# Kernel tuning notes

Hardware: AMD Instinct MI355X
Metric: run time of the kernel (lower is better)

## Reference

```python
import jax, jax.numpy as jnp
import numpy as np

B, S, D_MODEL = 4, 2048, 1024
N_HEAD, D_K, D_V = 16, 64, 64
LN_EPS = 1e-5


def setup_inputs() -> dict:
    key = jax.random.key(0)
    ks = jax.random.split(key, 8)
    std_qk = np.sqrt(2.0 / (D_MODEL + D_K)).astype(np.float32)
    std_v = np.sqrt(2.0 / (D_MODEL + D_V)).astype(np.float32)
    return {
        "q": jax.random.normal(ks[0], (B, S, D_MODEL), dtype=jnp.float32),
        "k": jax.random.normal(ks[1], (B, S, D_MODEL), dtype=jnp.float32),
        "v": jax.random.normal(ks[2], (B, S, D_MODEL), dtype=jnp.float32),
        "attn_mask": jax.random.randint(ks[3], (B, 1, S), 0, 2) > 0,
        # torch Linear weights: (out_features, in_features)
        "w_q": jax.random.normal(ks[4], (N_HEAD * D_K, D_MODEL), dtype=jnp.float32) * std_qk,
        "w_k": jax.random.normal(ks[5], (N_HEAD * D_K, D_MODEL), dtype=jnp.float32) * std_qk,
        "w_v": jax.random.normal(ks[6], (N_HEAD * D_V, D_MODEL), dtype=jnp.float32) * std_v,
        "w_fc": jax.random.normal(ks[7], (D_MODEL, N_HEAD * D_V), dtype=jnp.float32) * np.sqrt(2.0 / (D_MODEL + N_HEAD * D_V)).astype(np.float32),
        "ln_gamma": jnp.ones((D_MODEL,), dtype=jnp.float32),
        "ln_beta": jnp.zeros((D_MODEL,), dtype=jnp.float32),
    }


def _layer_norm(x, gamma, beta):
    mu = jnp.mean(x, axis=-1, keepdims=True)
    var = jnp.mean(jnp.square(x - mu), axis=-1, keepdims=True)
    return (x - mu) * jax.lax.rsqrt(var + LN_EPS) * gamma + beta


def reference(q, k, v, attn_mask, w_q, w_k, w_v, w_fc, ln_gamma, ln_beta):
    b, sq, _ = q.shape
    residual = q
    qh = (q @ w_q.T).reshape(b, sq, N_HEAD, D_K)          # [b,sq,h,dk]
    kh = (k @ w_k.T).reshape(b, -1, N_HEAD, D_K)          # [b,sk,h,dk]
    vh = (v @ w_v.T).reshape(b, -1, N_HEAD, D_V)          # [b,sk,h,dv]
    temperature = jnp.asarray(np.power(D_K, 0.5), dtype=q.dtype)
    scores = jnp.einsum("bqhd,bkhd->bhqk", qh, kh) / temperature
    # attn_mask: [b,1,sk] key-padding mask, True = masked
    scores = jnp.where(attn_mask[:, None, :, :], jnp.asarray(-1e6, scores.dtype), scores)
    attn = jax.nn.softmax(scores, axis=-1)                 # dropout is identity in eval
    out = jnp.einsum("bhqk,bkhd->bqhd", attn, vh).reshape(b, sq, N_HEAD * D_V)
    out = out @ w_fc.T
    out = _layer_norm(out + residual, ln_gamma, ln_beta)
    return out, attn
```

## Files before the change

kernel.cpp:

```cpp
#include <hip/hip_runtime.h>
#include <cstdint>
#include <cstddef>

#define B_  4
#define S_  2048
#define DM_ 1024
#define H_  16

typedef _Float16 h8 __attribute__((ext_vector_type(8)));
typedef _Float16 h4 __attribute__((ext_vector_type(4)));
typedef float f32x4 __attribute__((ext_vector_type(4)));

#define MFMA16(A_, B2_, C_) __builtin_amdgcn_mfma_f32_16x16x32_f16((A_), (B2_), (C_), 0, 0, 0)

__device__ __forceinline__ void gload_lds16(const void* g, void* l) {
  __builtin_amdgcn_global_load_lds(
      (const __attribute__((address_space(1))) unsigned int*)g,
      (__attribute__((address_space(3))) unsigned int*)l, 16, 0, 0);
}

template <int MODE, int A16>
__global__ __launch_bounds__(256, 2)
void gemm_bt(const void* __restrict__ Ap, const void* __restrict__ Wp,
             void* __restrict__ outp, int M, int N, int K) {
  __shared__ _Float16 As[128 * 32];
  __shared__ _Float16 Bs[128 * 32];
  const int tid = threadIdx.x;
  const int w = tid >> 6, lane = tid & 63;
  const int g = lane >> 4, li = lane & 15;
  const int wr = w >> 1, wc = w & 1;
  const int mBase = blockIdx.y * 128, nBase = blockIdx.x * 128;

  f32x4 acc[4][4] = {};

  _Float16* lA = As + w * 1024;
  _Float16* lB = Bs + w * 1024;

  const _Float16* gA16 =
      (const _Float16*)Ap + (size_t)(mBase + w * 32 + (lane >> 2)) * K + (lane & 3) * 8;
  const float* gA32 =
      (const float*)Ap + (size_t)(mBase + w * 32 + (lane >> 3)) * K + (lane & 7) * 4;
  const float* gW =
      (const float*)Wp + (size_t)(nBase + w * 32 + (lane >> 3)) * K + (lane & 7) * 4;

  for (int kt = 0; kt < K; kt += 32) {
    if (kt) __syncthreads();
    if constexpr (A16) {
      gload_lds16(gA16 + kt, lA);
      gload_lds16(gA16 + kt + (size_t)16 * K, lA + 512);
    } else {
#pragma unroll
      for (int it = 0; it < 4; ++it) {
        f32x4 v = *(const f32x4*)(gA32 + kt + (size_t)(it * 8) * K);
        h4 o;
        o[0] = (_Float16)v[0]; o[1] = (_Float16)v[1];
        o[2] = (_Float16)v[2]; o[3] = (_Float16)v[3];
        *(h4*)&lA[(it * 8 + (lane >> 3)) * 32 + (lane & 7) * 4] = o;
      }
    }
#pragma unroll
    for (int it = 0; it < 4; ++it) {
      f32x4 v = *(const f32x4*)(gW + kt + (size_t)(it * 8) * K);
      h4 o;
      o[0] = (_Float16)v[0]; o[1] = (_Float16)v[1];
      o[2] = (_Float16)v[2]; o[3] = (_Float16)v[3];
      *(h4*)&lB[(it * 8 + (lane >> 3)) * 32 + (lane & 7) * 4] = o;
    }
    __syncthreads();
    h8 af[4], bf[4];
#pragma unroll
    for (int t = 0; t < 4; ++t) af[t] = *(const h8*)&As[(wr * 64 + t * 16 + li) * 32 + g * 8];
#pragma unroll
    for (int u = 0; u < 4; ++u) bf[u] = *(const h8*)&Bs[(wc * 64 + u * 16 + li) * 32 + g * 8];
#pragma unroll
    for (int t = 0; t < 4; ++t)
#pragma unroll
      for (int u = 0; u < 4; ++u) acc[t][u] = MFMA16(af[t], bf[u], acc[t][u]);
  }

#pragma unroll
  for (int t = 0; t < 4; ++t) {
    const int grow0 = mBase + wr * 64 + t * 16 + g * 4;
#pragma unroll
    for (int u = 0; u < 4; ++u) {
      const int gcol = nBase + wc * 64 + u * 16 + li;
      if (MODE == 2) {
        float* o = (float*)outp;
#pragma unroll
        for (int r = 0; r < 4; ++r) o[(size_t)(grow0 + r) * N + gcol] = acc[t][u][r];
      } else if (MODE == 0) {
        _Float16* o = (_Float16*)outp;
        const int hh = gcol >> 6, d = gcol & 63;
#pragma unroll
        for (int r = 0; r < 4; ++r) {
          const int grow = grow0 + r;
          const int bb = grow >> 11, ss = grow & 2047;
          o[((size_t)((bb * H_ + hh) * S_ + ss)) * 64 + d] = (_Float16)acc[t][u][r];
        }
      } else {
        _Float16* o = (_Float16*)outp;
        const int hh = gcol >> 6, d = gcol & 63;
        const int bb = grow0 >> 11, ss = grow0 & 2047;
        h4 vv;
#pragma unroll
        for (int r = 0; r < 4; ++r) vv[r] = (_Float16)acc[t][u][r];
        *(h4*)&o[((size_t)((bb * H_ + hh) * 64 + d)) * S_ + ss] = vv;
      }
    }
  }
}

__global__ __launch_bounds__(256, 6)
void qk1_kernel(const _Float16* __restrict__ qh, const _Float16* __restrict__ kh,
                const int* __restrict__ mask, float* __restrict__ rlws) {
  __shared__ _Float16 sbias[S_];
  __shared__ __align__(16) _Float16 Ks[128 * 72];
  const int tid = threadIdx.x;
  const int w = tid >> 6, lane = tid & 63;
  const int g = lane >> 4, li = lane & 15;
  const int id = blockIdx.x;
  const int hh = id & 15, bb = (id >> 4) & 3, qt = id >> 6;
  const size_t bhS = ((size_t)bb * H_ + hh) * S_;
  const _Float16* khb = kh + bhS * 64;

  {
    const int4* mi = (const int4*)(mask + (size_t)bb * S_);
    int4 m0 = mi[tid * 2];
    int4 m1 = mi[tid * 2 + 1];
    _Float16* d = sbias + tid * 8;
    d[0] = m0.x ? (_Float16)-60000.f : (_Float16)-10.f;
    d[1] = m0.y ? (_Float16)-60000.f : (_Float16)-10.f;
    d[2] = m0.z ? (_Float16)-60000.f : (_Float16)-10.f;
    d[3] = m0.w ? (_Float16)-60000.f : (_Float16)-10.f;
    d[4] = m1.x ? (_Float16)-60000.f : (_Float16)-10.f;
    d[5] = m1.y ? (_Float16)-60000.f : (_Float16)-10.f;
    d[6] = m1.z ? (_Float16)-60000.f : (_Float16)-10.f;
    d[7] = m1.w ? (_Float16)-60000.f : (_Float16)-10.f;
  }

  h8 aq[2][2];
#pragma unroll
  for (int t = 0; t < 2; ++t) {
    const _Float16* qp = qh + (bhS + qt * 128 + w * 32 + t * 16 + li) * 64;
    aq[t][0] = *(const h8*)(qp + g * 8);
    aq[t][1] = *(const h8*)(qp + 32 + g * 8);
  }

  const int srow = tid >> 3;
  const int ssl = tid & 7;

  float l[2][4] = {};
  for (int kc = 0; kc < 16; ++kc) {
    __syncthreads();
#pragma unroll
    for (int rnd = 0; rnd < 4; ++rnd) {
      const int row = rnd * 32 + srow;
      const h8 kv = *(const h8*)(khb + (size_t)(kc * 128 + row) * 64 + ssl * 8);
      *(h8*)&Ks[row * 72 + ssl * 8] = kv;
    }
    __syncthreads();
    for (int kk = 0; kk < 8; ++kk) {
      const int krow = kk * 16 + li;
      const h8 bk0 = *(const h8*)&Ks[krow * 72 + g * 8];
      const h8 bk1 = *(const h8*)&Ks[krow * 72 + 32 + g * 8];
      const float bias = (float)sbias[kc * 128 + krow];
#pragma unroll
      for (int t = 0; t < 2; ++t) {
        f32x4 a = {0.f, 0.f, 0.f, 0.f};
        a = MFMA16(aq[t][0], bk0, a);
        a = MFMA16(aq[t][1], bk1, a);
#pragma unroll
        for (int r = 0; r < 4; ++r) l[t][r] += __expf(fmaf(a[r], 0.125f, bias));
      }
    }
  }

#pragma unroll
  for (int t = 0; t < 2; ++t)
#pragma unroll
    for (int r = 0; r < 4; ++r) {
      float s = l[t][r];
      s += __shfl_xor(s, 1);
      s += __shfl_xor(s, 2);
      s += __shfl_xor(s, 4);
      s += __shfl_xor(s, 8);
      if (li == 0)
        rlws[bhS + qt * 128 + w * 32 + t * 16 + g * 4 + r] = 1.0f / s;
    }
}

__global__ __launch_bounds__(256, 2)
void qk2_kernel(const _Float16* __restrict__ qh, const _Float16* __restrict__ kh,
                const _Float16* __restrict__ vt, const int* __restrict__ mask,
                const float* __restrict__ rlws, float* __restrict__ attn_out,
                _Float16* __restrict__ ctx) {
  __shared__ _Float16 sbias[S_];
  __shared__ __align__(16) _Float16 Pst[4][16 * 264];
  __shared__ __align__(16) _Float16 Ku[256 * 72];
  const int tid = threadIdx.x;
  const int w = tid >> 6, lane = tid & 63;
  const int g = lane >> 4, li = lane & 15;
  const int id = blockIdx.x;
  const int hh = id & 15, bb = (id >> 4) & 3, qt = id >> 6;
  const size_t bhS = ((size_t)bb * H_ + hh) * S_;
  const _Float16* khb = kh + bhS * 64;
  const _Float16* Vbg = vt + bhS * 64;

  {
    const int4* mi = (const int4*)(mask + (size_t)bb * S_);
    int4 m0 = mi[tid * 2];
    int4 m1 = mi[tid * 2 + 1];
    _Float16* d = sbias + tid * 8;
    d[0] = m0.x ? (_Float16)-60000.f : (_Float16)-10.f;
    d[1] = m0.y ? (_Float16)-60000.f : (_Float16)-10.f;
    d[2] = m0.z ? (_Float16)-60000.f : (_Float16)-10.f;
    d[3] = m0.w ? (_Float16)-60000.f : (_Float16)-10.f;
    d[4] = m1.x ? (_Float16)-60000.f : (_Float16)-10.f;
    d[5] = m1.y ? (_Float16)-60000.f : (_Float16)-10.f;
    d[6] = m1.z ? (_Float16)-60000.f : (_Float16)-10.f;
    d[7] = m1.w ? (_Float16)-60000.f : (_Float16)-10.f;
  }

  h8 aq[2][2];
  float rl[2][4];
#pragma unroll
  for (int t = 0; t < 2; ++t) {
    const _Float16* qp = qh + (bhS + qt * 128 + w * 32 + t * 16 + li) * 64;
    aq[t][0] = *(const h8*)(qp + g * 8);
    aq[t][1] = *(const h8*)(qp + 32 + g * 8);
#pragma unroll
    for (int r = 0; r < 4; ++r)
      rl[t][r] = rlws[bhS + qt * 128 + w * 32 + t * 16 + g * 4 + r];
  }

  float* ab = attn_out + (bhS + qt * 128) * S_;
  _Float16* Pw = &Pst[w][0];
  f32x4 acc[2][4] = {};

  const int ksrow = tid >> 3;
  const int kssl = tid & 7;
  const int vsrow = tid >> 5;
  const int vssl = tid & 31;

  for (int kc = 0; kc < 8; ++kc) {
#pragma unroll
    for (int t = 0; t < 2; ++t) {
      __syncthreads();
#pragma unroll
      for (int rnd = 0; rnd < 8; ++rnd) {
        const int row = rnd * 32 + ksrow;
        const h8 kv = *(const h8*)(khb + (size_t)(kc * 256 + row) * 64 + kssl * 8);
        *(h8*)&Ku[row * 72 + kssl * 8] = kv;
      }
      __syncthreads();
      for (int kk = 0; kk < 16; ++kk) {
        const int krow = kk * 16 + li;
        const h8 bk0 = *(const h8*)&Ku[krow * 72 + g * 8];
        const h8 bk1 = *(const h8*)&Ku[krow * 72 + 32 + g * 8];
        const float bias = (float)sbias[kc * 256 + krow];
        f32x4 a = {0.f, 0.f, 0.f, 0.f};
        a = MFMA16(aq[t][0], bk0, a);
        a = MFMA16(aq[t][1], bk1, a);
#pragma unroll
        for (int r = 0; r < 4; ++r) {
          Pw[(g * 4 + r) * 264 + krow] =
              (_Float16)(__expf(fmaf(a[r], 0.125f, bias)) * rl[t][r]);
        }
      }
#pragma unroll
      for (int rr = 0; rr < 16; ++rr) {
        const h4 p = *(const h4*)&Pw[rr * 264 + lane * 4];
        f32x4 o;
        o[0] = (float)p[0]; o[1] = (float)p[1];
        o[2] = (float)p[2]; o[3] = (float)p[3];
        __builtin_nontemporal_store(
            o, (f32x4*)(ab + (size_t)(w * 32 + t * 16 + rr) * S_ + kc * 256 + lane * 4));
      }
      __syncthreads();
#pragma unroll
      for (int rnd = 0; rnd < 8; ++rnd) {
        const int row = rnd * 8 + vsrow;
        const h8 vv = *(const h8*)(Vbg + (size_t)row * S_ + kc * 256 + vssl * 8);
        *(h8*)&Ku[row * 264 + vssl * 8] = vv;
      }
      __syncthreads();
#pragma unroll
      for (int ks = 0; ks < 8; ++ks) {
        const h8 pa = *(const h8*)&Pw[li * 264 + ks * 32 + g * 8];
#pragma unroll
        for (int u = 0; u < 4; ++u) {
          const h8 bf = *(const h8*)&Ku[(u * 16 + li) * 264 + ks * 32 + g * 8];
          acc[t][u] = MFMA16(pa, bf, acc[t][u]);
        }
      }
    }
  }

  _Float16* cb = ctx + ((size_t)bb * S_ + qt * 128 + w * 32 + g * 4) * DM_ + hh * 64 + li;
#pragma unroll
  for (int t = 0; t < 2; ++t)
#pragma unroll
    for (int u = 0; u < 4; ++u)
#pragma unroll
      for (int r = 0; r < 4; ++r)
        cb[(size_t)(t * 16 + r) * DM_ + u * 16] = (_Float16)acc[t][u][r];
}

__global__ __launch_bounds__(256)
void ln_kernel(const float* __restrict__ fc, const float* __restrict__ resid,
               const float* __restrict__ gamma, const float* __restrict__ beta,
               float* __restrict__ out) {
  __shared__ float red[8];
  const int row = blockIdx.x;
  const int t = threadIdx.x, w = t >> 6, lane = t & 63;
  const f32x4 xv = *(const f32x4*)(fc + (size_t)row * DM_ + t * 4);
  const f32x4 rv = *(const f32x4*)(resid + (size_t)row * DM_ + t * 4);
  float x0 = xv[0] + rv[0], x1 = xv[1] + rv[1], x2 = xv[2] + rv[2], x3 = xv[3] + rv[3];
  float s = x0 + x1 + x2 + x3;
#pragma unroll
  for (int off = 1; off < 64; off <<= 1) s += __shfl_xor(s, off);
  if (lane == 0) red[w] = s;
  __syncthreads();
  const float mu = (red[0] + red[1] + red[2] + red[3]) * (1.0f / (float)DM_);
  const float d0 = x0 - mu, d1 = x1 - mu, d2 = x2 - mu, d3 = x3 - mu;
  float sq = d0 * d0 + d1 * d1 + d2 * d2 + d3 * d3;
#pragma unroll
  for (int off = 1; off < 64; off <<= 1) sq += __shfl_xor(sq, off);
  if (lane == 0) red[4 + w] = sq;
  __syncthreads();
  const float inv = rsqrtf((red[4] + red[5] + red[6] + red[7]) * (1.0f / (float)DM_) + 1e-5f);
  const f32x4 gv = *(const f32x4*)(gamma + t * 4);
  const f32x4 bv = *(const f32x4*)(beta + t * 4);
  f32x4 o;
  o[0] = d0 * inv * gv[0] + bv[0];
  o[1] = d1 * inv * gv[1] + bv[1];
  o[2] = d2 * inv * gv[2] + bv[2];
  o[3] = d3 * inv * gv[3] + bv[3];
  *(f32x4*)(out + (size_t)row * DM_ + t * 4) = o;
}

extern "C" void kernel_launch(void* const* d_in, const int* in_sizes, int n_in,
                              void* d_out, int out_size, void* d_ws, size_t ws_size,
                              hipStream_t stream) {
  const float* q = (const float*)d_in[0];
  const float* k = (const float*)d_in[1];
  const float* v = (const float*)d_in[2];
  const int* mask = (const int*)d_in[3];
  const float* wq = (const float*)d_in[4];
  const float* wk = (const float*)d_in[5];
  const float* wv = (const float*)d_in[6];
  const float* wfc = (const float*)d_in[7];
  const float* gamma = (const float*)d_in[8];
  const float* beta = (const float*)d_in[9];

  float* out0 = (float*)d_out;
  float* attn = out0 + (size_t)B_ * S_ * DM_;
  float* rlws = out0;

  char* ws = (char*)d_ws;
  _Float16* qhp = (_Float16*)(ws + (0ull << 20));
  _Float16* khp = (_Float16*)(ws + (16ull << 20));
  _Float16* vtp = (_Float16*)(ws + (32ull << 20));
  _Float16* ctxp = (_Float16*)(ws + (48ull << 20));
  float* fcp = (float*)(ws + (0ull << 20));

  dim3 gg(DM_ / 128, B_ * S_ / 128);
  gemm_bt<0, 0><<<gg, 256, 0, stream>>>(q, wq, qhp, B_ * S_, DM_, DM_);
  gemm_bt<0, 0><<<gg, 256, 0, stream>>>(k, wk, khp, B_ * S_, DM_, DM_);
  gemm_bt<1, 0><<<gg, 256, 0, stream>>>(v, wv, vtp, B_ * S_, DM_, DM_);

  qk1_kernel<<<dim3(1024), 256, 0, stream>>>(qhp, khp, mask, rlws);
  qk2_kernel<<<dim3(1024), 256, 0, stream>>>(qhp, khp, vtp, mask, rlws, attn, ctxp);

  gemm_bt<2, 1><<<gg, 256, 0, stream>>>(ctxp, wfc, fcp, B_ * S_, DM_, DM_);

  ln_kernel<<<B_ * S_, 256, 0, stream>>>(fcp, q, gamma, beta, out0);
}
```

Measured before the change: 529.4 us.

## Restructure attention second pass into 128-key chunks with register-prefetched K/V

The second attention kernel now walks keys in 128-wide chunks instead of 256. It loads K once per chunk and shares it across both query sub-tiles, rather than reloading K and V separately for each sub-tile. The next chunk's K and the current chunk's V are fetched into registers ahead of use, so global load latency overlaps with the exp/store work, and the number of barriers per chunk drops. Smaller chunks and padded strides cut LDS use and may change bank conflicts and occupancy, at the cost of more loop iterations and extra registers for the prefetch.

Result: slower. 551.7 us (+4.2%).

```diff
diff --git a/kernel.cpp b/kernel.cpp
--- a/kernel.cpp
+++ b/kernel.cpp
@@ -195,8 +195,9 @@
                 const float* __restrict__ rlws, float* __restrict__ attn_out,
                 _Float16* __restrict__ ctx) {
   __shared__ _Float16 sbias[S_];
-  __shared__ __align__(16) _Float16 Pst[4][16 * 264];
-  __shared__ __align__(16) _Float16 Ku[256 * 72];
+  __shared__ __align__(16) _Float16 Ks[128 * 88];
+  __shared__ __align__(16) _Float16 Vs[64 * 168];
+  __shared__ __align__(16) _Float16 Pst[4][16 * 168];
   const int tid = threadIdx.x;
   const int w = tid >> 6, lane = tid & 63;
   const int g = lane >> 4, li = lane & 15;
@@ -237,61 +238,98 @@
   _Float16* Pw = &Pst[w][0];
   f32x4 acc[2][4] = {};
 
-  const int ksrow = tid >> 3;
-  const int kssl = tid & 7;
-  const int vsrow = tid >> 5;
-  const int vssl = tid & 31;
-
-  for (int kc = 0; kc < 8; ++kc) {
-#pragma unroll
-    for (int t = 0; t < 2; ++t) {
-      __syncthreads();
-#pragma unroll
-      for (int rnd = 0; rnd < 8; ++rnd) {
-        const int row = rnd * 32 + ksrow;
-        const h8 kv = *(const h8*)(khb + (size_t)(kc * 256 + row) * 64 + kssl * 8);
-        *(h8*)&Ku[row * 72 + kssl * 8] = kv;
+  const int krow_s = tid >> 3, kslot = tid & 7;
+  const int vrow_s = tid >> 4, vslot = tid & 15;
+  const int srl = lane >> 5;
+  const int scl = (lane & 31) * 4;
+
+  h8 kpre[4], vpre[4];
+#pragma unroll
+  for (int rnd = 0; rnd < 4; ++rnd)
+    kpre[rnd] = *(const h8*)(khb + (size_t)(rnd * 32 + krow_s) * 64 + kslot * 8);
+
+  for (int kc = 0; kc < 16; ++kc) {
+    __syncthreads();
+#pragma unroll
+    for (int rnd = 0; rnd < 4; ++rnd)
+      *(h8*)&Ks[(rnd * 32 + krow_s) * 88 + kslot * 8] = kpre[rnd];
+    __syncthreads();
+
+    for (int kk = 0; kk < 8; ++kk) {
+      const int krow = kk * 16 + li;
+      const h8 bk0 = *(const h8*)&Ks[krow * 88 + g * 8];
+      const h8 bk1 = *(const h8*)&Ks[krow * 88 + 32 + g * 8];
+      const float bias = (float)sbias[kc * 128 + krow];
+      f32x4 a = {0.f, 0.f, 0.f, 0.f};
+      a = MFMA16(aq[0][0], bk0, a);
+      a = MFMA16(aq[0][1], bk1, a);
+#pragma unroll
+      for (int r = 0; r < 4; ++r)
+        Pw[(g * 4 + r) * 168 + krow] =
+            (_Float16)(__expf(fmaf(a[r], 0.125f, bias)) * rl[0][r]);
+    }
+#pragma unroll
+    for (int rnd = 0; rnd < 4; ++rnd)
+      vpre[rnd] = *(const h8*)(Vbg + (size_t)(rnd * 16 + vrow_s) * S_ + kc * 128 + vslot * 8);
+#pragma unroll
+    for (int rr = 0; rr < 8; ++rr) {
+      const int row2 = rr * 2 + srl;
+      const h4 p = *(const h4*)&Pw[row2 * 168 + scl];
+      f32x4 o;
+      o[0] = (float)p[0]; o[1] = (float)p[1];
+      o[2] = (float)p[2]; o[3] = (float)p[3];
+      __builtin_nontemporal_store(
+          o, (f32x4*)(ab + (size_t)(w * 32 + row2) * S_ + kc * 128 + scl));
+    }
+#pragma unroll
+    for (int rnd = 0; rnd < 4; ++rnd)
+      *(h8*)&Vs[(rnd * 16 + vrow_s) * 168 + vslot * 8] = vpre[rnd];
+    __syncthreads();
+#pragma unroll
+    for (int ks = 0; ks < 4; ++ks) {
+      const h8 pa = *(const h8*)&Pw[li * 168 + ks * 32 + g * 8];
+#pragma unroll
+      for (int u = 0; u < 4; ++u) {
+        const h8 bf = *(const h8*)&Vs[(u * 16 + li) * 168 + ks * 32 + g * 8];
+        acc[0][u] = MFMA16(pa, bf, acc[0][u]);
       }
-      __syncthreads();
-      for (int kk = 0; kk < 16; ++kk) {
-        const int krow = kk * 16 + li;
-        const h8 bk0 = *(const h8*)&Ku[krow * 72 + g * 8];
-        const h8 bk1 = *(const h8*)&Ku[krow * 72 + 32 + g * 8];
-        const float bias = (float)sbias[kc * 256 + krow];
-        f32x4 a = {0.f, 0.f, 0.f, 0.f};
-        a = MFMA16(aq[t][0], bk0, a);
-        a = MFMA16(aq[t][1], bk1, a);
-#pragma unroll
-        for (int r = 0; r < 4; ++r) {
-          Pw[(g * 4 + r) * 264 + krow] =
-              (_Float16)(__expf(fmaf(a[r], 0.125f, bias)) * rl[t][r]);
-        }
-      }
-#pragma unroll
-      for (int rr = 0; rr < 16; ++rr) {
-        const h4 p = *(const h4*)&Pw[rr * 264 + lane * 4];
-        f32x4 o;
-        o[0] = (float)p[0]; o[1] = (float)p[1];
-        o[2] = (float)p[2]; o[3] = (float)p[3];
-        __builtin_nontemporal_store(
-            o, (f32x4*)(ab + (size_t)(w * 32 + t * 16 + rr) * S_ + kc * 256 + lane * 4));
-      }
-      __syncthreads();
-#pragma unroll
-      for (int rnd = 0; rnd < 8; ++rnd) {
-        const int row = rnd * 8 + vsrow;
-        const h8 vv = *(const h8*)(Vbg + (size_t)row * S_ + kc * 256 + vssl * 8);
-        *(h8*)&Ku[row * 264 + vssl * 8] = vv;
-      }
-      __syncthreads();
-#pragma unroll
-      for (int ks = 0; ks < 8; ++ks) {
-        const h8 pa = *(const h8*)&Pw[li * 264 + ks * 32 + g * 8];
-#pragma unroll
-        for (int u = 0; u < 4; ++u) {
-          const h8 bf = *(const h8*)&Ku[(u * 16 + li) * 264 + ks * 32 + g * 8];
-          acc[t][u] = MFMA16(pa, bf, acc[t][u]);
-        }
+    }
+
+    for (int kk = 0; kk < 8; ++kk) {
+      const int krow = kk * 16 + li;
+      const h8 bk0 = *(const h8*)&Ks[krow * 88 + g * 8];
+      const h8 bk1 = *(const h8*)&Ks[krow * 88 + 32 + g * 8];
+      const float bias = (float)sbias[kc * 128 + krow];
+      f32x4 a = {0.f, 0.f, 0.f, 0.f};
+      a = MFMA16(aq[1][0], bk0, a);
+      a = MFMA16(aq[1][1], bk1, a);
+#pragma unroll
+      for (int r = 0; r < 4; ++r)
+        Pw[(g * 4 + r) * 168 + krow] =
+            (_Float16)(__expf(fmaf(a[r], 0.125f, bias)) * rl[1][r]);
+    }
+    const int kcn = (kc + 1 < 16) ? kc + 1 : 0;
+#pragma unroll
+    for (int rnd = 0; rnd < 4; ++rnd)
+      kpre[rnd] =
+          *(const h8*)(khb + (size_t)(kcn * 128 + rnd * 32 + krow_s) * 64 + kslot * 8);
+#pragma unroll
+    for (int rr = 0; rr < 8; ++rr) {
+      const int row2 = rr * 2 + srl;
+      const h4 p = *(const h4*)&Pw[row2 * 168 + scl];
+      f32x4 o;
+      o[0] = (float)p[0]; o[1] = (float)p[1];
+      o[2] = (float)p[2]; o[3] = (float)p[3];
+      __builtin_nontemporal_store(
+          o, (f32x4*)(ab + (size_t)(w * 32 + 16 + row2) * S_ + kc * 128 + scl));
+    }
+#pragma unroll
+    for (int ks = 0; ks < 4; ++ks) {
+      const h8 pa = *(const h8*)&Pw[li * 168 + ks * 32 + g * 8];
+#pragma unroll
+      for (int u = 0; u < 4; ++u) {
+        const h8 bf = *(const h8*)&Vs[(u * 16 + li) * 168 + ks * 32 + g * 8];
+        acc[1][u] = MFMA16(pa, bf, acc[1][u]);
       }
     }
   }
```

## Shrink qk2 key tile to 64 and stage K and V together

Applied to the files above, without the earlier changes.

Restructures the attention-probability and P·V kernel to process keys in 64-wide chunks, loading the K and V tiles once per chunk for both query sub-tiles instead of reloading K per sub-tile with separate V staging. This cuts shared memory per block (smaller P scratch and K/V buffers) and raises the launch-bounds occupancy target from 2 to 4 blocks per CU, aiming to hide latency better and remove redundant K loads and syncs. In exchange there are four times as many chunk iterations, each with its own barriers, and the attn stores are narrower per row.

After: 530.5 us. No clear change (+0.2%).

```diff
diff --git a/kernel.cpp b/kernel.cpp
--- a/kernel.cpp
+++ b/kernel.cpp
@@ -189,14 +189,15 @@
     }
 }
 
-__global__ __launch_bounds__(256, 2)
+__global__ __launch_bounds__(256, 4)
 void qk2_kernel(const _Float16* __restrict__ qh, const _Float16* __restrict__ kh,
                 const _Float16* __restrict__ vt, const int* __restrict__ mask,
                 const float* __restrict__ rlws, float* __restrict__ attn_out,
                 _Float16* __restrict__ ctx) {
   __shared__ _Float16 sbias[S_];
-  __shared__ __align__(16) _Float16 Pst[4][16 * 264];
-  __shared__ __align__(16) _Float16 Ku[256 * 72];
+  __shared__ __align__(16) _Float16 Ks[64 * 72];
+  __shared__ __align__(16) _Float16 Vs[64 * 72];
+  __shared__ __align__(16) _Float16 Pst[4][16 * 72];
   const int tid = threadIdx.x;
   const int w = tid >> 6, lane = tid & 63;
   const int g = lane >> 4, li = lane & 15;
@@ -237,59 +238,55 @@
   _Float16* Pw = &Pst[w][0];
   f32x4 acc[2][4] = {};
 
-  const int ksrow = tid >> 3;
-  const int kssl = tid & 7;
-  const int vsrow = tid >> 5;
-  const int vssl = tid & 31;
-
-  for (int kc = 0; kc < 8; ++kc) {
+  const int srow = tid >> 3;
+  const int ssl = tid & 7;
+  const int strow = lane >> 4;
+  const int stcol = (lane & 15) * 4;
+
+  for (int kc = 0; kc < 32; ++kc) {
+    __syncthreads();
+#pragma unroll
+    for (int rnd = 0; rnd < 2; ++rnd) {
+      const int row = rnd * 32 + srow;
+      const h8 kv = *(const h8*)(khb + (size_t)(kc * 64 + row) * 64 + ssl * 8);
+      *(h8*)&Ks[row * 72 + ssl * 8] = kv;
+      const h8 vv = *(const h8*)(Vbg + (size_t)row * S_ + kc * 64 + ssl * 8);
+      *(h8*)&Vs[row * 72 + ssl * 8] = vv;
+    }
+    __syncthreads();
+
 #pragma unroll
     for (int t = 0; t < 2; ++t) {
-      __syncthreads();
-#pragma unroll
-      for (int rnd = 0; rnd < 8; ++rnd) {
-        const int row = rnd * 32 + ksrow;
-        const h8 kv = *(const h8*)(khb + (size_t)(kc * 256 + row) * 64 + kssl * 8);
-        *(h8*)&Ku[row * 72 + kssl * 8] = kv;
-      }
-      __syncthreads();
-      for (int kk = 0; kk < 16; ++kk) {
+#pragma unroll
+      for (int kk = 0; kk < 4; ++kk) {
         const int krow = kk * 16 + li;
-        const h8 bk0 = *(const h8*)&Ku[krow * 72 + g * 8];
-        const h8 bk1 = *(const h8*)&Ku[krow * 72 + 32 + g * 8];
-        const float bias = (float)sbias[kc * 256 + krow];
+        const h8 bk0 = *(const h8*)&Ks[krow * 72 + g * 8];
+        const h8 bk1 = *(const h8*)&Ks[krow * 72 + 32 + g * 8];
+        const float bias = (float)sbias[kc * 64 + krow];
         f32x4 a = {0.f, 0.f, 0.f, 0.f};
         a = MFMA16(aq[t][0], bk0, a);
         a = MFMA16(aq[t][1], bk1, a);
 #pragma unroll
-        for (int r = 0; r < 4; ++r) {
-          Pw[(g * 4 + r) * 264 + krow] =
+        for (int r = 0; r < 4; ++r)
+          Pw[(g * 4 + r) * 72 + krow] =
               (_Float16)(__expf(fmaf(a[r], 0.125f, bias)) * rl[t][r]);
-        }
-      }
-#pragma unroll
-      for (int rr = 0; rr < 16; ++rr) {
-        const h4 p = *(const h4*)&Pw[rr * 264 + lane * 4];
+      }
+#pragma unroll
+      for (int rr = 0; rr < 4; ++rr) {
+        const int row4 = rr * 4 + strow;
+        const h4 p = *(const h4*)&Pw[row4 * 72 + stcol];
         f32x4 o;
         o[0] = (float)p[0]; o[1] = (float)p[1];
         o[2] = (float)p[2]; o[3] = (float)p[3];
         __builtin_nontemporal_store(
-            o, (f32x4*)(ab + (size_t)(w * 32 + t * 16 + rr) * S_ + kc * 256 + lane * 4));
-      }
-      __syncthreads();
-#pragma unroll
-      for (int rnd = 0; rnd < 8; ++rnd) {
-        const int row = rnd * 8 + vsrow;
-        const h8 vv = *(const h8*)(Vbg + (size_t)row * S_ + kc * 256 + vssl * 8);
-        *(h8*)&Ku[row * 264 + vssl * 8] = vv;
-      }
-      __syncthreads();
-#pragma unroll
-      for (int ks = 0; ks < 8; ++ks) {
-        const h8 pa = *(const h8*)&Pw[li * 264 + ks * 32 + g * 8];
+            o, (f32x4*)(ab + (size_t)(w * 32 + t * 16 + row4) * S_ + kc * 64 + stcol));
+      }
+#pragma unroll
+      for (int ks = 0; ks < 2; ++ks) {
+        const h8 pa = *(const h8*)&Pw[li * 72 + ks * 32 + g * 8];
 #pragma unroll
         for (int u = 0; u < 4; ++u) {
-          const h8 bf = *(const h8*)&Ku[(u * 16 + li) * 264 + ks * 32 + g * 8];
+          const h8 bf = *(const h8*)&Vs[(u * 16 + li) * 72 + ks * 32 + g * 8];
           acc[t][u] = MFMA16(pa, bf, acc[t][u]);
         }
       }
```
